# Kernel tuning notes

Measured on AMD Instinct MI355X. Metric: run time of the kernel, lower is better.

## Reference

```python
import jax, jax.numpy as jnp
import numpy as np

N_NODES = 100000
N_EDGES = 1600000
IN_CH = 64
OUT_CH = 32
HEADS = 4
NEG_SLOPE = 0.2


def setup_inputs() -> dict:
    key = jax.random.key(0)
    k = jax.random.split(key, 6)
    x = jax.random.normal(k[0], (N_NODES, IN_CH), dtype=jnp.float32)
    edge_index = jax.random.randint(k[1], (2, N_EDGES), 0, N_NODES, dtype=jnp.int32)
    W = jax.random.normal(k[2], (IN_CH, HEADS * OUT_CH), dtype=jnp.float32) * 0.1
    att_src = jax.random.normal(k[3], (1, HEADS, OUT_CH), dtype=jnp.float32) * 0.1
    att_dst = jax.random.normal(k[4], (1, HEADS, OUT_CH), dtype=jnp.float32) * 0.1
    bias = jnp.zeros((HEADS * OUT_CH,), dtype=jnp.float32)
    return {"x": x, "edge_index": edge_index, "W": W,
            "att_src": att_src, "att_dst": att_dst, "bias": bias}


def reference(x, edge_index, W, att_src, att_dst, bias):
    N = x.shape[0]
    H, C = att_src.shape[1], att_src.shape[2]
    # GATConv defaults: add self loops
    loop = jnp.arange(N, dtype=edge_index.dtype)
    src = jnp.concatenate([edge_index[0], loop])  # [E+N]
    dst = jnp.concatenate([edge_index[1], loop])  # [E+N]
    # linear transform -> [N, H, C]
    h = (x @ W).reshape(N, H, C)
    # per-node attention halves: [N, H]
    a_src = jnp.sum(h * att_src, axis=-1)
    a_dst = jnp.sum(h * att_dst, axis=-1)
    # edge scores with LeakyReLU: [E+N, H]
    e = jax.nn.leaky_relu(a_src[src] + a_dst[dst], negative_slope=NEG_SLOPE)
    # segment softmax over destination nodes (numerically stable)
    m = jax.ops.segment_max(e, dst, num_segments=N)           # [N, H]
    m = jnp.where(jnp.isfinite(m), m, 0.0)
    ex = jnp.exp(e - m[dst])                                   # [E+N, H]
    denom = jax.ops.segment_sum(ex, dst, num_segments=N)      # [N, H]
    alpha = ex / (denom[dst] + 1e-16)                          # [E+N, H]
    # scatter-aggregate weighted source features -> [N, H, C]
    out = jax.ops.segment_sum(h[src] * alpha[:, :, None], dst, num_segments=N)
    out = out.reshape(N, H * C) + bias
    return jax.nn.log_softmax(out, axis=1)
```

## Files before the change

kernel.cpp:

```cpp
#include <hip/hip_runtime.h>
#include <hip/hip_bf16.h>

#define IN_CH 64
#define HC 128
#define NHEAD 4
#define NEG 0.2f
#define CAPB 64
#define NB 250
#define BWID 400
#define CAP2 8192
#define CH1 4096
#define VPT 8

typedef short s16x8 __attribute__((ext_vector_type(8)));
typedef float f32x4 __attribute__((ext_vector_type(4)));

__device__ __forceinline__ float leaky(float v) { return fmaxf(v, NEG * v); }
__device__ __forceinline__ unsigned short f2bf(float f) {
    unsigned int u = __float_as_uint(f);
    u += 0x7fff + ((u >> 16) & 1);
    return (unsigned short)(u >> 16);
}
__device__ __forceinline__ float4 add4(float4 a, float4 b) {
    return make_float4(a.x + b.x, a.y + b.y, a.z + b.z, a.w + b.w);
}
__device__ __forceinline__ float4 leaky4(float4 v) {
    return make_float4(leaky(v.x), leaky(v.y), leaky(v.z), leaky(v.w));
}
__device__ __forceinline__ float4 exp4(float4 v) {
    return make_float4(__expf(v.x), __expf(v.y), __expf(v.z), __expf(v.w));
}
__device__ __forceinline__ float comp4(float4 v, int i) {
    float r = v.x;
    r = (i == 1) ? v.y : r;
    r = (i == 2) ? v.z : r;
    r = (i == 3) ? v.w : r;
    return r;
}

#define ACC8(al, hv)                                                  \
    do {                                                              \
        acc[0] = fmaf((al), __uint_as_float((hv).x << 16), acc[0]);   \
        acc[1] = fmaf((al), __uint_as_float((hv).x & 0xffff0000u), acc[1]); \
        acc[2] = fmaf((al), __uint_as_float((hv).y << 16), acc[2]);   \
        acc[3] = fmaf((al), __uint_as_float((hv).y & 0xffff0000u), acc[3]); \
        acc[4] = fmaf((al), __uint_as_float((hv).z << 16), acc[4]);   \
        acc[5] = fmaf((al), __uint_as_float((hv).z & 0xffff0000u), acc[5]); \
        acc[6] = fmaf((al), __uint_as_float((hv).w << 16), acc[6]);   \
        acc[7] = fmaf((al), __uint_as_float((hv).w & 0xffff0000u), acc[7]); \
    } while (0)

__global__ void __launch_bounds__(512, 4) k_front(
        const float* __restrict__ x, const float* __restrict__ W,
        const float* __restrict__ att_src, const float* __restrict__ att_dst,
        unsigned short* __restrict__ h_bf, float* __restrict__ a_src,
        float* __restrict__ a_dst,
        const int* __restrict__ src, const int* __restrict__ dst,
        int* __restrict__ bcnt, int* __restrict__ pairs,
        int E, int N, int NXB) {
    __shared__ union {
        struct { unsigned short xs[128][72]; unsigned short wt[144][72]; } xf;
        struct { int hist[NB]; int scanbuf[256]; int startb[NB]; int gbase[NB];
                 int lbuf[CH1]; int gposb[CH1]; } bn;
    } sm;
    const int t = threadIdx.x;
    const int r3 = blockIdx.x % 3;

    if (r3 < 2) {
        const int xb = (blockIdx.x / 3) * 2 + r3;
        if (xb >= NXB) return;
        const int rowbase_blk = xb * 128;

        for (int idx = t; idx < (IN_CH * HC) / 4; idx += 512) {
            const float4 v = ((const float4*)W)[idx];
            const int k = idx >> 5;
            const int c0 = (idx & 31) * 4;
            sm.xf.wt[c0 + 0][k] = f2bf(v.x);
            sm.xf.wt[c0 + 1][k] = f2bf(v.y);
            sm.xf.wt[c0 + 2][k] = f2bf(v.z);
            sm.xf.wt[c0 + 3][k] = f2bf(v.w);
        }
        for (int idx = t; idx < 16 * 64; idx += 512) {
            const int j = idx >> 6, k = idx & 63;
            float v = 0.f;
            if (j < 8) {
                const int h = j & 3;
                const float* att = (j < 4) ? att_src : att_dst;
#pragma unroll
                for (int c = 0; c < 32; ++c)
                    v += W[k * HC + h * 32 + c] * att[h * 32 + c];
            }
            sm.xf.wt[128 + j][k] = f2bf(v);
        }
        for (int idx = t; idx < (128 * IN_CH) / 4; idx += 512) {
            const int row = idx >> 4;
            const int c0 = (idx & 15) * 4;
            const int grow = min(rowbase_blk + row, N - 1);
            const float4 v = ((const float4*)(x + (size_t)grow * IN_CH))[idx & 15];
            const unsigned int p0 = (unsigned int)f2bf(v.x) | ((unsigned int)f2bf(v.y) << 16);
            const unsigned int p1 = (unsigned int)f2bf(v.z) | ((unsigned int)f2bf(v.w) << 16);
            *(uint2*)&sm.xf.xs[row][c0] = make_uint2(p0, p1);
        }
        __syncthreads();

        const int lane = t & 63;
        const int w = t >> 6;
        const int rbase = w * 16;
        const int lr = lane & 15, lq = lane >> 4;

        f32x4 acc[9];
#pragma unroll
        for (int n = 0; n < 9; ++n) acc[n] = (f32x4){0.f, 0.f, 0.f, 0.f};

#pragma unroll
        for (int ks = 0; ks < 2; ++ks) {
            const s16x8 a0 = *(const s16x8*)&sm.xf.xs[rbase + lr][ks * 32 + lq * 8];
#pragma unroll
            for (int n = 0; n < 9; ++n) {
                const s16x8 b = *(const s16x8*)&sm.xf.wt[n * 16 + lr][ks * 32 + lq * 8];
                acc[n] = __builtin_amdgcn_mfma_f32_16x16x32_bf16(a0, b, acc[n], 0, 0, 0);
            }
        }

#pragma unroll
        for (int j = 0; j < 4; ++j) {
            const int grow = rowbase_blk + rbase + lq * 4 + j;
            if (grow >= N) continue;
#pragma unroll
            for (int n = 0; n < 8; ++n)
                h_bf[(size_t)grow * HC + n * 16 + lr] = f2bf(acc[n][j]);
            const float av = acc[8][j];
            if (lr < 4) a_src[grow * NHEAD + lr] = av;
            else if (lr < 8) a_dst[grow * NHEAD + (lr - 4)] = av;
        }
    } else {
        const int bb = blockIdx.x / 3;
        const int base = bb * CH1;
        const int cnt = min(CH1, E - base);

        for (int i = t; i < NB; i += 512) sm.bn.hist[i] = 0;
        __syncthreads();

        int pk[VPT]; int rb[VPT];
#pragma unroll
        for (int k = 0; k < VPT; ++k) {
            const int idx = base + k * 512 + t;
            if (idx < E) {
                const int s = src[idx], d = dst[idx];
                const int b = d / BWID;
                const int dl = d - b * BWID;
                pk[k] = (dl << 17) | s;
                const int rank = atomicAdd(&sm.bn.hist[b], 1);
                rb[k] = (b << 16) | rank;
            } else {
                pk[k] = 0; rb[k] = -1;
            }
        }
        __syncthreads();

        if (t < 256) sm.bn.scanbuf[t] = (t < NB) ? sm.bn.hist[t] : 0;
        __syncthreads();
        for (int off = 1; off < 256; off <<= 1) {
            int add = 0;
            if (t < 256 && t >= off) add = sm.bn.scanbuf[t - off];
            __syncthreads();
            if (t < 256) sm.bn.scanbuf[t] += add;
            __syncthreads();
        }
        if (t < NB) {
            const int h = sm.bn.hist[t];
            sm.bn.startb[t] = sm.bn.scanbuf[t] - h;
            sm.bn.gbase[t] = (h > 0) ? atomicAdd(&bcnt[t * 16], h) : 0;
        }
        __syncthreads();

#pragma unroll
        for (int k = 0; k < VPT; ++k) {
            if (rb[k] >= 0) {
                const int b = rb[k] >> 16;
                const int rank = rb[k] & 0xffff;
                const int lpos = sm.bn.startb[b] + rank;
                const int gp = sm.bn.gbase[b] + rank;
                sm.bn.lbuf[lpos] = pk[k];
                sm.bn.gposb[lpos] = (gp < CAP2) ? (b * CAP2 + gp) : -1;
            }
        }
        __syncthreads();

        for (int i = t; i < cnt; i += 512) {
            const int g = sm.bn.gposb[i];
            if (g >= 0) pairs[g] = sm.bn.lbuf[i];
        }
    }
}

__global__ void __launch_bounds__(512) k_fill(
        const int* __restrict__ bcnt, const int* __restrict__ pairs,
        int* __restrict__ srcbuf, int* __restrict__ rowstart,
        int* __restrict__ deg) {
    const int b = blockIdx.x;
    const int t = threadIdx.x;
    __shared__ int scnt[BWID];
    __shared__ int sstart[BWID];
    __shared__ int cur[BWID];
    __shared__ int scan2[512];
    __shared__ int slist[CAP2];
    __shared__ int sbase;

    int part = 0;
    for (int i = t; i < b; i += 512) part += min(bcnt[i * 16], CAP2);
    scan2[t] = part; __syncthreads();
    for (int off = 256; off > 0; off >>= 1) {
        if (t < off) scan2[t] += scan2[t + off];
        __syncthreads();
    }
    if (t == 0) sbase = scan2[0];

    for (int i = t; i < BWID; i += 512) scnt[i] = 0;
    __syncthreads();

    const int mc = min(bcnt[b * 16], CAP2);
    const int pb = b * CAP2;

    for (int i = t; i < mc; i += 512)
        atomicAdd(&scnt[pairs[pb + i] >> 17], 1);
    __syncthreads();

    scan2[t] = (t < BWID) ? scnt[t] : 0;
    __syncthreads();
    for (int off = 1; off < 512; off <<= 1) {
        const int add = (t >= off) ? scan2[t - off] : 0;
        __syncthreads();
        scan2[t] += add;
        __syncthreads();
    }
    if (t < BWID) {
        const int ex = scan2[t] - scnt[t];
        sstart[t] = ex; cur[t] = ex;
        rowstart[b * BWID + t] = sbase + ex;
        deg[b * BWID + t] = scnt[t];
    }
    __syncthreads();

    for (int i = t; i < mc; i += 512) {
        const int e = pairs[pb + i];
        const int p = atomicAdd(&cur[e >> 17], 1);
        slist[p] = e & 0x1ffff;
    }
    __syncthreads();

    for (int i = t; i < mc; i += 512) srcbuf[sbase + i] = slist[i];
}

__global__ void __launch_bounds__(256) k_node(
        const int* __restrict__ deg_, const int* __restrict__ rowstart,
        const int* __restrict__ srcbuf,
        const float* __restrict__ a_src, const float* __restrict__ a_dst,
        const unsigned short* __restrict__ h_bf, const float* __restrict__ bias,
        float* __restrict__ out, int N) {
    const int slot = threadIdx.x >> 4;
    const int l = threadIdx.x & 15;
    int n = blockIdx.x * 16 + slot;
    n = min(n, N - 1);
    const int deg = deg_[n];
    const int start = rowstart[n];
    const int dcap = min(deg, CAPB);

    __shared__ int s_src[16][CAPB];

    const float4 ad4  = *(const float4*)(a_dst + n * NHEAD);
    const float4 asn4 = *(const float4*)(a_src + n * NHEAD);

    float4 sum4 = make_float4(0.f, 0.f, 0.f, 0.f);
    for (int j = l; j < dcap; j += 16) {
        const int s = srcbuf[start + j];
        s_src[slot][j] = s;
        const float4 a = *(const float4*)(a_src + s * NHEAD);
        sum4 = add4(sum4, exp4(leaky4(add4(a, ad4))));
    }
    for (int j = CAPB + l; j < deg; j += 16) {
        const int s = srcbuf[start + j];
        const float4 a = *(const float4*)(a_src + s * NHEAD);
        sum4 = add4(sum4, exp4(leaky4(add4(a, ad4))));
    }
#pragma unroll
    for (int off = 1; off < 16; off <<= 1) {
        sum4.x += __shfl_xor(sum4.x, off, 64);
        sum4.y += __shfl_xor(sum4.y, off, 64);
        sum4.z += __shfl_xor(sum4.z, off, 64);
        sum4.w += __shfl_xor(sum4.w, off, 64);
    }
    const float4 self4 = exp4(leaky4(add4(asn4, ad4)));
    sum4 = add4(sum4, self4);
    const float4 r4v = make_float4(1.f / (sum4.x + 1e-16f), 1.f / (sum4.y + 1e-16f),
                                   1.f / (sum4.z + 1e-16f), 1.f / (sum4.w + 1e-16f));

    __builtin_amdgcn_wave_barrier();

    const int hd = l >> 2;
    const float rsel = comp4(r4v, hd);
    const float adh  = comp4(ad4, hd);
    float acc[8];
#pragma unroll
    for (int k = 0; k < 8; ++k) acc[k] = 0.f;

    int j = 0;
    for (; j + 2 <= dcap; j += 2) {
        const int s0 = s_src[slot][j];
        const int s1 = s_src[slot][j + 1];
        const float a0 = a_src[s0 * NHEAD + hd];
        const float a1 = a_src[s1 * NHEAD + hd];
        const uint4 h0 = *(const uint4*)(h_bf + (size_t)s0 * HC + l * 8);
        const uint4 h1 = *(const uint4*)(h_bf + (size_t)s1 * HC + l * 8);
        const float al0 = __expf(leaky(a0 + adh));
        const float al1 = __expf(leaky(a1 + adh));
        ACC8(al0, h0);
        ACC8(al1, h1);
    }
    if (j < dcap) {
        const int s0 = s_src[slot][j];
        const float al0 = __expf(leaky(a_src[s0 * NHEAD + hd] + adh));
        const uint4 h0 = *(const uint4*)(h_bf + (size_t)s0 * HC + l * 8);
        ACC8(al0, h0);
    }
    for (int jj = CAPB; jj < deg; ++jj) {
        const int s = srcbuf[start + jj];
        const float al = __expf(leaky(a_src[s * NHEAD + hd] + adh));
        const uint4 hv = *(const uint4*)(h_bf + (size_t)s * HC + l * 8);
        ACC8(al, hv);
    }
    {
        const float als = comp4(self4, hd);
        const uint4 hv = *(const uint4*)(h_bf + (size_t)n * HC + l * 8);
        ACC8(als, hv);
    }

    const float4 b0 = *(const float4*)(bias + l * 8);
    const float4 b1 = *(const float4*)(bias + l * 8 + 4);
    acc[0] = acc[0] * rsel + b0.x; acc[1] = acc[1] * rsel + b0.y;
    acc[2] = acc[2] * rsel + b0.z; acc[3] = acc[3] * rsel + b0.w;
    acc[4] = acc[4] * rsel + b1.x; acc[5] = acc[5] * rsel + b1.y;
    acc[6] = acc[6] * rsel + b1.z; acc[7] = acc[7] * rsel + b1.w;

    float mxv = fmaxf(fmaxf(fmaxf(acc[0], acc[1]), fmaxf(acc[2], acc[3])),
                      fmaxf(fmaxf(acc[4], acc[5]), fmaxf(acc[6], acc[7])));
#pragma unroll
    for (int off = 1; off < 16; off <<= 1) mxv = fmaxf(mxv, __shfl_xor(mxv, off, 64));
    float se = 0.f;
#pragma unroll
    for (int k = 0; k < 8; ++k) se += __expf(acc[k] - mxv);
#pragma unroll
    for (int off = 1; off < 16; off <<= 1) se += __shfl_xor(se, off, 64);
    const float lse = mxv + __logf(se);

    float* op = out + (size_t)n * HC + l * 8;
    *(float4*)op = make_float4(acc[0] - lse, acc[1] - lse, acc[2] - lse, acc[3] - lse);
    *(float4*)(op + 4) = make_float4(acc[4] - lse, acc[5] - lse, acc[6] - lse, acc[7] - lse);
}

extern "C" void kernel_launch(void* const* d_in, const int* in_sizes, int n_in,
                              void* d_out, int out_size, void* d_ws, size_t ws_size,
                              hipStream_t stream) {
    const float* x       = (const float*)d_in[0];
    const int*   ei      = (const int*)d_in[1];
    const float* W       = (const float*)d_in[2];
    const float* att_src = (const float*)d_in[3];
    const float* att_dst = (const float*)d_in[4];
    const float* bias    = (const float*)d_in[5];
    float* out = (float*)d_out;

    const int N = in_sizes[0] / IN_CH;
    const int E = in_sizes[1] / 2;
    const int* src = ei;
    const int* dst = ei + E;

    char* wsb = (char*)d_ws;
    unsigned short* h_bf = (unsigned short*)wsb;    wsb += (size_t)N * HC * 2;
    float* a_src  = (float*)wsb;                    wsb += (size_t)N * NHEAD * 4;
    float* a_dst  = (float*)wsb;                    wsb += (size_t)N * NHEAD * 4;
    int*   bcnt   = (int*)wsb;                      wsb += (size_t)NB * 16 * 4;
    int*   pairs  = (int*)wsb;                      wsb += (size_t)NB * CAP2 * 4;
    int*   srcbuf = (int*)wsb;                      wsb += (size_t)E * 4;
    int*   rowstart = (int*)wsb;                    wsb += (size_t)N * 4;
    int*   deg    = (int*)wsb;                      wsb += (size_t)N * 4;

    const int NXB = (N + 127) / 128;
    const int NBB = (E + CH1 - 1) / CH1;

    hipMemsetAsync(bcnt, 0, (size_t)NB * 16 * 4, stream);

    k_front<<<NBB * 3, 512, 0, stream>>>(x, W, att_src, att_dst,
                                         h_bf, a_src, a_dst,
                                         src, dst, bcnt, pairs, E, N, NXB);
    k_fill<<<NB, 512, 0, stream>>>(bcnt, pairs, srcbuf, rowstart, deg);
    k_node<<<(N + 15) / 16, 256, 0, stream>>>(deg, rowstart, srcbuf,
                                              a_src, a_dst,
                                              (const unsigned short*)h_bf, bias, out, N);
}
```

Before: 208.8 us.

## Use power-of-two dst buckets and cache edge exp weights in shared memory

Buckets destination nodes into 782 power-of-two-wide buckets of 128, so bucket and local index come from shifts instead of a division. The front-end scan and the fill kernel are resized to match, with the fill kernel now running 256 threads per block. The node kernel stores the per-edge exp attention values computed in the softmax-denominator pass in shared memory and reuses them in aggregation, avoiding a second a_src gather and exp. The inline cap on in-shared-memory edges drops from 64 to 32, so high-degree nodes fall back to the slower serial global path more often, and the smaller per-bucket capacity raises overflow risk.

```diff
diff --git a/kernel.cpp b/kernel.cpp
--- a/kernel.cpp
+++ b/kernel.cpp
@@ -5,10 +5,10 @@
 #define HC 128
 #define NHEAD 4
 #define NEG 0.2f
-#define CAPB 64
-#define NB 250
-#define BWID 400
-#define CAP2 8192
+#define CAPB 32
+#define BWID 128
+#define NB 782
+#define CAP2 2560
 #define CH1 4096
 #define VPT 8
 
@@ -60,7 +60,7 @@
         int E, int N, int NXB) {
     __shared__ union {
         struct { unsigned short xs[128][72]; unsigned short wt[144][72]; } xf;
-        struct { int hist[NB]; int scanbuf[256]; int startb[NB]; int gbase[NB];
+        struct { int hist[NB]; int scanbuf[1024]; int startb[NB]; int gbase[NB];
                  int lbuf[CH1]; int gposb[CH1]; } bn;
     } sm;
     const int t = threadIdx.x;
@@ -147,8 +147,8 @@
             const int idx = base + k * 512 + t;
             if (idx < E) {
                 const int s = src[idx], d = dst[idx];
-                const int b = d / BWID;
-                const int dl = d - b * BWID;
+                const int b = d >> 7;
+                const int dl = d & 127;
                 pk[k] = (dl << 17) | s;
                 const int rank = atomicAdd(&sm.bn.hist[b], 1);
                 rb[k] = (b << 16) | rank;
@@ -158,19 +158,21 @@
         }
         __syncthreads();
 
-        if (t < 256) sm.bn.scanbuf[t] = (t < NB) ? sm.bn.hist[t] : 0;
-        __syncthreads();
-        for (int off = 1; off < 256; off <<= 1) {
-            int add = 0;
-            if (t < 256 && t >= off) add = sm.bn.scanbuf[t - off];
+        sm.bn.scanbuf[t] = (t < NB) ? sm.bn.hist[t] : 0;
+        sm.bn.scanbuf[t + 512] = (t + 512 < NB) ? sm.bn.hist[t + 512] : 0;
+        __syncthreads();
+        for (int off = 1; off < 1024; off <<= 1) {
+            const int a0 = (t >= off) ? sm.bn.scanbuf[t - off] : 0;
+            const int a1 = (t + 512 >= off) ? sm.bn.scanbuf[t + 512 - off] : 0;
             __syncthreads();
-            if (t < 256) sm.bn.scanbuf[t] += add;
+            sm.bn.scanbuf[t] += a0;
+            sm.bn.scanbuf[t + 512] += a1;
             __syncthreads();
         }
-        if (t < NB) {
-            const int h = sm.bn.hist[t];
-            sm.bn.startb[t] = sm.bn.scanbuf[t] - h;
-            sm.bn.gbase[t] = (h > 0) ? atomicAdd(&bcnt[t * 16], h) : 0;
+        for (int i = t; i < NB; i += 512) {
+            const int h = sm.bn.hist[i];
+            sm.bn.startb[i] = sm.bn.scanbuf[i] - h;
+            sm.bn.gbase[i] = (h > 0) ? atomicAdd(&bcnt[i * 16], h) : 0;
         }
         __syncthreads();
 
@@ -194,62 +196,63 @@
     }
 }
 
-__global__ void __launch_bounds__(512) k_fill(
+__global__ void __launch_bounds__(256) k_fill(
         const int* __restrict__ bcnt, const int* __restrict__ pairs,
         int* __restrict__ srcbuf, int* __restrict__ rowstart,
-        int* __restrict__ deg) {
+        int* __restrict__ deg, int N) {
     const int b = blockIdx.x;
     const int t = threadIdx.x;
     __shared__ int scnt[BWID];
-    __shared__ int sstart[BWID];
     __shared__ int cur[BWID];
-    __shared__ int scan2[512];
+    __shared__ int scan2[256];
     __shared__ int slist[CAP2];
-    __shared__ int sbase;
+    __shared__ int sbase_s;
 
     int part = 0;
-    for (int i = t; i < b; i += 512) part += min(bcnt[i * 16], CAP2);
+    for (int i = t; i < b; i += 256) part += min(bcnt[i * 16], CAP2);
     scan2[t] = part; __syncthreads();
-    for (int off = 256; off > 0; off >>= 1) {
+    for (int off = 128; off > 0; off >>= 1) {
         if (t < off) scan2[t] += scan2[t + off];
         __syncthreads();
     }
-    if (t == 0) sbase = scan2[0];
-
-    for (int i = t; i < BWID; i += 512) scnt[i] = 0;
+    if (t == 0) sbase_s = scan2[0];
+    if (t < BWID) scnt[t] = 0;
     __syncthreads();
 
     const int mc = min(bcnt[b * 16], CAP2);
     const int pb = b * CAP2;
 
-    for (int i = t; i < mc; i += 512)
+    for (int i = t; i < mc; i += 256)
         atomicAdd(&scnt[pairs[pb + i] >> 17], 1);
     __syncthreads();
 
-    scan2[t] = (t < BWID) ? scnt[t] : 0;
+    if (t < BWID) scan2[t] = scnt[t];
     __syncthreads();
-    for (int off = 1; off < 512; off <<= 1) {
-        const int add = (t >= off) ? scan2[t - off] : 0;
-        __syncthreads();
-        scan2[t] += add;
+    for (int off = 1; off < BWID; off <<= 1) {
+        const int add = (t >= off && t < BWID) ? scan2[t - off] : 0;
+        __syncthreads();
+        if (t < BWID) scan2[t] += add;
         __syncthreads();
     }
     if (t < BWID) {
         const int ex = scan2[t] - scnt[t];
-        sstart[t] = ex; cur[t] = ex;
-        rowstart[b * BWID + t] = sbase + ex;
-        deg[b * BWID + t] = scnt[t];
+        cur[t] = ex;
+        const int n = b * BWID + t;
+        if (n < N) {
+            rowstart[n] = sbase_s + ex;
+            deg[n] = scnt[t];
+        }
     }
     __syncthreads();
 
-    for (int i = t; i < mc; i += 512) {
+    for (int i = t; i < mc; i += 256) {
         const int e = pairs[pb + i];
         const int p = atomicAdd(&cur[e >> 17], 1);
         slist[p] = e & 0x1ffff;
     }
     __syncthreads();
 
-    for (int i = t; i < mc; i += 512) srcbuf[sbase + i] = slist[i];
+    for (int i = t; i < mc; i += 256) srcbuf[sbase_s + i] = slist[i];
 }
 
 __global__ void __launch_bounds__(256) k_node(
@@ -266,7 +269,8 @@
     const int start = rowstart[n];
     const int dcap = min(deg, CAPB);
 
-    __shared__ int s_src[16][CAPB];
+    __shared__ float s_ex[16][CAPB + 1][NHEAD];
+    __shared__ int   s_src[16][CAPB + 1];
 
     const float4 ad4  = *(const float4*)(a_dst + n * NHEAD);
     const float4 asn4 = *(const float4*)(a_src + n * NHEAD);
@@ -276,7 +280,9 @@
         const int s = srcbuf[start + j];
         s_src[slot][j] = s;
         const float4 a = *(const float4*)(a_src + s * NHEAD);
-        sum4 = add4(sum4, exp4(leaky4(add4(a, ad4))));
+        const float4 e4 = exp4(leaky4(add4(a, ad4)));
+        *(float4*)&s_ex[slot][j][0] = e4;
+        sum4 = add4(sum4, e4);
     }
     for (int j = CAPB + l; j < deg; j += 16) {
         const int s = srcbuf[start + j];
@@ -308,19 +314,17 @@
     for (; j + 2 <= dcap; j += 2) {
         const int s0 = s_src[slot][j];
         const int s1 = s_src[slot][j + 1];
-        const float a0 = a_src[s0 * NHEAD + hd];
-        const float a1 = a_src[s1 * NHEAD + hd];
         const uint4 h0 = *(const uint4*)(h_bf + (size_t)s0 * HC + l * 8);
         const uint4 h1 = *(const uint4*)(h_bf + (size_t)s1 * HC + l * 8);
-        const float al0 = __expf(leaky(a0 + adh));
-        const float al1 = __expf(leaky(a1 + adh));
+        const float al0 = s_ex[slot][j][hd];
+        const float al1 = s_ex[slot][j + 1][hd];
         ACC8(al0, h0);
         ACC8(al1, h1);
     }
     if (j < dcap) {
         const int s0 = s_src[slot][j];
-        const float al0 = __expf(leaky(a_src[s0 * NHEAD + hd] + adh));
         const uint4 h0 = *(const uint4*)(h_bf + (size_t)s0 * HC + l * 8);
+        const float al0 = s_ex[slot][j][hd];
         ACC8(al0, h0);
     }
     for (int jj = CAPB; jj < deg; ++jj) {
@@ -392,7 +396,7 @@
     k_front<<<NBB * 3, 512, 0, stream>>>(x, W, att_src, att_dst,
                                          h_bf, a_src, a_dst,
                                          src, dst, bcnt, pairs, E, N, NXB);
-    k_fill<<<NB, 512, 0, stream>>>(bcnt, pairs, srcbuf, rowstart, deg);
+    k_fill<<<NB, 256, 0, stream>>>(bcnt, pairs, srcbuf, rowstart, deg, N);
     k_node<<<(N + 15) / 16, 256, 0, stream>>>(deg, rowstart, srcbuf,
                                               a_src, a_dst,
                                               (const unsigned short*)h_bf, bias, out, N);
```

New measurement: 211.1 us. Within noise of the previous version (+1.1%).
